# Kernel optimization log

Measured on AMD Instinct MI355X. Metric: run time of the kernel, lower is better.

## Reference

```python
import jax, jax.numpy as jnp
import numpy as np

H = 256          # hidden_channels
NP, NJ, NC = 8192, 8192, 4096  # person / job_posting / company node counts
EA, EW, EP = 262144, 131072, 131072  # edge counts per relation


def _gcn(x_src, W, b, edge_index, num_src, num_dst):
    """Bipartite GCNConv: h = x_src @ W; out[dst] = sum_e norm_e * h[src_e] + b,
    norm = deg_out(src)^-1/2 * deg_in(dst)^-1/2 (symmetric GCN normalization)."""
    h = x_src @ W                                # [num_src, H]
    row, col = edge_index[0], edge_index[1]
    ones = jnp.ones(row.shape[0], dtype=h.dtype)
    deg_src = jax.ops.segment_sum(ones, row, num_segments=num_src)
    deg_dst = jax.ops.segment_sum(ones, col, num_segments=num_dst)
    dis_src = jnp.where(deg_src > 0, jax.lax.rsqrt(jnp.maximum(deg_src, 1e-12)), 0.0)
    dis_dst = jnp.where(deg_dst > 0, jax.lax.rsqrt(jnp.maximum(deg_dst, 1e-12)), 0.0)
    norm = dis_src[row] * dis_dst[col]           # [E]
    out = jax.ops.segment_sum(h[row] * norm[:, None], col, num_segments=num_dst)
    return out + b


def setup_inputs() -> dict:
    key = jax.random.key(0)
    ks = jax.random.split(key, 12)
    s = 1.0 / np.sqrt(H)
    return {
        "x_person":  jax.random.normal(ks[0], (NP, H), jnp.float32),
        "x_job":     jax.random.normal(ks[1], (NJ, H), jnp.float32),
        "x_company": jax.random.normal(ks[2], (NC, H), jnp.float32),
        "ei_applied": jax.random.randint(ks[3], (2, EA), 0, 8192, jnp.int64 if jax.config.read('jax_enable_x64') else jnp.int32),
        "ei_worked":  jax.random.randint(ks[4], (2, EW), 0, 4096, jnp.int64 if jax.config.read('jax_enable_x64') else jnp.int32),
        "ei_posted":  jax.random.randint(ks[5], (2, EP), 0, 4096, jnp.int64 if jax.config.read('jax_enable_x64') else jnp.int32),
        "W_aj": jax.random.normal(ks[6], (H, H), jnp.float32) * s,
        "b_aj": jnp.zeros((H,), jnp.float32),
        "W_wa": jax.random.normal(ks[7], (H, H), jnp.float32) * s,
        "b_wa": jnp.zeros((H,), jnp.float32),
        "W_pb": jax.random.normal(ks[8], (H, H), jnp.float32) * s,
        "b_pb": jnp.zeros((H,), jnp.float32),
    }


def reference(x_person, x_job, x_company, ei_applied, ei_worked, ei_posted,
              W_aj, b_aj, W_wa, b_wa, W_pb, b_pb):
    Np, Nj, Nc = x_person.shape[0], x_job.shape[0], x_company.shape[0]
    # HeteroConv with aggr='sum': each dst type sums messages over its edge types
    job_emb = _gcn(x_person, W_aj, b_aj, ei_applied, Np, Nj)
    comp_emb = (_gcn(x_person, W_wa, b_wa, ei_worked, Np, Nc)
                + _gcn(x_job, W_pb, b_pb, ei_posted, Nj, Nc))  # computed but unused downstream
    del comp_emb
    person_emb = x_person  # 'person' is never a dst type; features pass through
    scores = jax.nn.sigmoid(person_emb @ job_emb.T)  # [Np, Nj]
    return scores
```

## Files before the change

### kernel.cpp

```cpp
#include <hip/hip_runtime.h>
#include <hip/hip_bf16.h>

#define HCH 256
#define NPN 8192
#define NJN 8192
#define EAE 262144
#define CAP 96

typedef _Float16 f16x8 __attribute__((ext_vector_type(8)));
typedef _Float16 f16x4 __attribute__((ext_vector_type(4)));
typedef float f32x4 __attribute__((ext_vector_type(4)));

typedef __attribute__((address_space(1))) void glb_void;
typedef __attribute__((address_space(3))) void lds_void;

#define WS_CUR   0
#define WS_DEG   32768
#define WS_CSR2  65536
#define WS_XH    3211264
#define WS_ZH    7405568
#define WS_GH    11599872
#define WS_WHT   15794176

__global__ void k_init(int* __restrict__ cnt, const float* __restrict__ W,
                       _Float16* __restrict__ WhT, const float* __restrict__ x,
                       _Float16* __restrict__ Xh) {
    int bid = blockIdx.x, t = threadIdx.x;
    if (bid < 64) {
        cnt[bid * 256 + t] = 0;
    } else if (bid < 320) {
        int idx = (bid - 64) * 256 + t;
        int n = idx >> 8, k = idx & 255;
        WhT[idx] = (_Float16)W[k * HCH + n];
    } else {
        int i = ((bid - 320) * 256 + t) * 4;
        float4 v = *(const float4*)(x + i);
        f16x4 h;
        h[0] = (_Float16)v.x; h[1] = (_Float16)v.y;
        h[2] = (_Float16)v.z; h[3] = (_Float16)v.w;
        *(f16x4*)(Xh + i) = h;
    }
}

__global__ void k_edge(const int* __restrict__ row, const int* __restrict__ col,
                       int* __restrict__ deg_src, int* __restrict__ cur,
                       int* __restrict__ csr2) {
    int e = blockIdx.x * 256 + threadIdx.x;
    int r = row[e], c = col[e];
    atomicAdd(&deg_src[r], 1);
    int p = atomicAdd(&cur[c], 1);
    if (p < CAP) csr2[c * CAP + p] = r;
}

__global__ __launch_bounds__(64)
void k_agg(const _Float16* __restrict__ Xh, const int* __restrict__ csr2,
           const int* __restrict__ cur, const int* __restrict__ deg_src,
           _Float16* __restrict__ Zh) {
    int j = blockIdx.x;
    int t = threadIdx.x;
    int degt = cur[j];
    int deg = degt > CAP ? CAP : degt;

    __shared__ int   sidx[CAP];
    __shared__ float sw[CAP];
    for (int b = t; b < deg; b += 64) {
        int s = csr2[j * CAP + b];
        sidx[b] = s;
        sw[b] = rsqrtf((float)deg_src[s]);
    }
    __syncthreads();

    float a0 = 0.f, a1 = 0.f, a2 = 0.f, a3 = 0.f;
    const _Float16* xb = Xh + t * 4;
    int e = 0;
    for (; e + 4 <= deg; e += 4) {
        int s0 = sidx[e], s1 = sidx[e + 1], s2 = sidx[e + 2], s3 = sidx[e + 3];
        float w0 = sw[e], w1 = sw[e + 1], w2 = sw[e + 2], w3 = sw[e + 3];
        f16x4 v0 = *(const f16x4*)(xb + (size_t)s0 * HCH);
        f16x4 v1 = *(const f16x4*)(xb + (size_t)s1 * HCH);
        f16x4 v2 = *(const f16x4*)(xb + (size_t)s2 * HCH);
        f16x4 v3 = *(const f16x4*)(xb + (size_t)s3 * HCH);
        a0 += w0 * (float)v0[0] + w1 * (float)v1[0] + w2 * (float)v2[0] + w3 * (float)v3[0];
        a1 += w0 * (float)v0[1] + w1 * (float)v1[1] + w2 * (float)v2[1] + w3 * (float)v3[1];
        a2 += w0 * (float)v0[2] + w1 * (float)v1[2] + w2 * (float)v2[2] + w3 * (float)v3[2];
        a3 += w0 * (float)v0[3] + w1 * (float)v1[3] + w2 * (float)v2[3] + w3 * (float)v3[3];
    }
    for (; e < deg; e++) {
        int s0 = sidx[e];
        float w0 = sw[e];
        f16x4 v0 = *(const f16x4*)(xb + (size_t)s0 * HCH);
        a0 += w0 * (float)v0[0]; a1 += w0 * (float)v0[1];
        a2 += w0 * (float)v0[2]; a3 += w0 * (float)v0[3];
    }
    f16x4 out;
    if (degt > 0) {
        float dd = rsqrtf((float)degt);
        out[0] = (_Float16)(a0 * dd); out[1] = (_Float16)(a1 * dd);
        out[2] = (_Float16)(a2 * dd); out[3] = (_Float16)(a3 * dd);
    } else {
        out[0] = out[1] = out[2] = out[3] = (_Float16)0.f;
    }
    *(f16x4*)(Zh + (size_t)j * HCH + t * 4) = out;
}

template <int TM, int TN>
__global__ __launch_bounds__(256, 2)
void k_gemm(const _Float16* __restrict__ A, const _Float16* __restrict__ Bt,
            const float* __restrict__ bias, _Float16* __restrict__ Cout, int Ncols) {
    constexpr int WM = TM / 2, WN = TN / 2;
    constexpr int MR = WM / 16, NR = WN / 16;
    constexpr int CHA = TM * 8 / 256;
    constexpr int CHB = TN * 8 / 256;
    constexpr int BOFF = TM * 128;

    __shared__ _Float16 sm[2][(TM + TN) * 64];

    int tid = threadIdx.x;
    int wid = tid >> 6, lane = tid & 63;

    int brow = blockIdx.y * TM;
    int bcol = blockIdx.x * TN;
    int wrow = (wid >> 1) * WM;
    int wcol = (wid & 1) * WN;

    f32x4 acc[MR][NR] = {};

    int lr = lane & 15;
    int kq = lane >> 4;

    auto stage = [&](int t, int b) {
        int k0 = t * 64;
#pragma unroll
        for (int i = 0; i < CHA; i++) {
            int wc0 = i * 256 + wid * 64;
            int c = wc0 + lane;
            int r = c >> 3, cc = c & 7;
            const char* ga = (const char*)A +
                (size_t)(brow + r) * (HCH * 2) + (size_t)(k0 + cc * 8) * 2;
            __builtin_amdgcn_global_load_lds(
                (glb_void*)ga, (lds_void*)((char*)sm[b] + wc0 * 16), 16, 0, 0);
        }
#pragma unroll
        for (int i = 0; i < CHB; i++) {
            int wc0 = i * 256 + wid * 64;
            int c = wc0 + lane;
            int r = c >> 3, cc = c & 7;
            const char* gb = (const char*)Bt +
                (size_t)(bcol + r) * (HCH * 2) + (size_t)(k0 + cc * 8) * 2;
            __builtin_amdgcn_global_load_lds(
                (glb_void*)gb, (lds_void*)((char*)sm[b] + BOFF + wc0 * 16), 16, 0, 0);
        }
    };

    stage(0, 0);
    __syncthreads();

    constexpr int NT = HCH / 64;
#pragma unroll
    for (int t = 0; t < NT; t++) {
        int cur = t & 1;
        if (t + 1 < NT) stage(t + 1, cur ^ 1);
        const char* base = (const char*)sm[cur];
#pragma unroll
        for (int kk = 0; kk < 64; kk += 32) {
            f16x8 af[MR], bfr[NR];
            int kbyte = (kk + kq * 8) * 2;
#pragma unroll
            for (int m = 0; m < MR; m++) {
                int r = wrow + m * 16 + lr;
                af[m] = *(const f16x8*)(base + r * 128 + kbyte);
            }
#pragma unroll
            for (int n = 0; n < NR; n++) {
                int r = wcol + n * 16 + lr;
                bfr[n] = *(const f16x8*)(base + BOFF + r * 128 + kbyte);
            }
#pragma unroll
            for (int m = 0; m < MR; m++)
#pragma unroll
                for (int n = 0; n < NR; n++)
                    acc[m][n] = __builtin_amdgcn_mfma_f32_16x16x32_f16(
                        af[m], bfr[n], acc[m][n], 0, 0, 0);
        }
        __syncthreads();
    }

    int rq = lane >> 4;
#pragma unroll
    for (int m = 0; m < MR; m++) {
#pragma unroll
        for (int n = 0; n < NR; n++) {
#pragma unroll
            for (int j = 0; j < 4; j++) {
                int gr = brow + wrow + m * 16 + rq * 4 + j;
                int gc = bcol + wcol + n * 16 + lr;
                float v = acc[m][n][j] + bias[gc];
                Cout[(size_t)gr * Ncols + gc] = (_Float16)v;
            }
        }
    }
}

#define G2_NW 32
__global__ __launch_bounds__(512, 1)
void k_gemm2(const _Float16* __restrict__ A, const _Float16* __restrict__ Bt,
             float* __restrict__ C) {
    __shared__ _Float16 smA[128 * HCH];
    __shared__ _Float16 smB[2][64 * HCH];
    __shared__ float    smC[128 * 64];

    int tid = threadIdx.x;
    int wid = tid >> 6, lane = tid & 63;
    int lr = lane & 15, kq = lane >> 4;

    int id = blockIdx.x;
    int xcd = id & 7, slot = id >> 3;
    int cg = xcd >> 1;
    int strip = slot + (xcd & 1) * 32;
    int brow = strip * 128;
    int bcol0 = cg * (64 * G2_NW);

    int wrow = (wid >> 1) * 32;
    int wcol = (wid & 1) * 32;

#pragma unroll
    for (int i = 0; i < 8; i++) {
        int wc0 = i * 512 + wid * 64;
        int c = wc0 + lane;
        int r = c >> 5, q = c & 31;
        int j = q ^ (r & 7);
        const char* ga = (const char*)(A + (size_t)(brow + r) * HCH + j * 8);
        __builtin_amdgcn_global_load_lds(
            (glb_void*)ga, (lds_void*)((char*)smA + wc0 * 16), 16, 0, 0);
    }
    auto stageB = [&](int t, int b) {
#pragma unroll
        for (int i = 0; i < 4; i++) {
            int wc0 = i * 512 + wid * 64;
            int c = wc0 + lane;
            int r = c >> 5, q = c & 31;
            int j = q ^ (r & 7);
            const char* gb = (const char*)(Bt +
                (size_t)(bcol0 + t * 64 + r) * HCH + j * 8);
            __builtin_amdgcn_global_load_lds(
                (glb_void*)gb, (lds_void*)((char*)smB[b] + wc0 * 16), 16, 0, 0);
        }
    };
    stageB(0, 0);
    __syncthreads();

    const char* sA = (const char*)smA;
    f16x8 areg[2][8];
#pragma unroll
    for (int m = 0; m < 2; m++) {
#pragma unroll
        for (int ks = 0; ks < 8; ks++) {
            int r = wrow + m * 16 + lr;
            int sb = ks * 4 + kq;
            areg[m][ks] = *(const f16x8*)(sA + r * 512 + ((sb ^ (r & 7)) << 4));
        }
    }

    for (int t = 0; t < G2_NW; t++) {
        int cb = t & 1;
        if (t + 1 < G2_NW) stageB(t + 1, cb ^ 1);
        __builtin_amdgcn_sched_barrier(0);
        const char* sB = (const char*)smB[cb];
        f32x4 acc[2][2] = {};
#pragma unroll
        for (int ks = 0; ks < 8; ks++) {
            f16x8 bf2[2];
            int sb = ks * 4 + kq;
#pragma unroll
            for (int n = 0; n < 2; n++) {
                int r = wcol + n * 16 + lr;
                bf2[n] = *(const f16x8*)(sB + r * 512 + ((sb ^ (r & 7)) << 4));
            }
#pragma unroll
            for (int m = 0; m < 2; m++)
#pragma unroll
                for (int n = 0; n < 2; n++)
                    acc[m][n] = __builtin_amdgcn_mfma_f32_16x16x32_f16(
                        bf2[n], areg[m][ks], acc[m][n], 0, 0, 0);
        }

#pragma unroll
        for (int m = 0; m < 2; m++) {
#pragma unroll
            for (int n = 0; n < 2; n++) {
                int row = wrow + m * 16 + lr;
                int ch = ((wcol + n * 16) >> 2) + kq;
                int sc = ch ^ (row & 7);
                *(f32x4*)(smC + row * 64 + sc * 4) = acc[m][n];
            }
        }
        asm volatile("s_waitcnt lgkmcnt(0)" ::: "memory");
        __builtin_amdgcn_s_barrier();
        __builtin_amdgcn_sched_barrier(0);

        int bcol = bcol0 + t * 64;
#pragma unroll
        for (int p = 0; p < 4; p++) {
            int flat = p * 512 + tid;
            int row = flat >> 4;
            int ch = flat & 15;
            int sc = ch ^ (row & 7);
            f32x4 v = *(const f32x4*)(smC + row * 64 + sc * 4);
            f32x4 o;
#pragma unroll
            for (int j = 0; j < 4; j++) {
                float e = __expf(-v[j]);
                o[j] = __builtin_amdgcn_rcpf(1.f + e);
            }
            __builtin_nontemporal_store(
                o, (f32x4*)(C + (size_t)(brow + row) * NJN + bcol + ch * 4));
        }

        if (t + 1 < G2_NW) {
            __builtin_amdgcn_sched_barrier(0);
            asm volatile("s_waitcnt vmcnt(4)" ::: "memory");
            __builtin_amdgcn_s_barrier();
            __builtin_amdgcn_sched_barrier(0);
        }
    }
}

extern "C" void kernel_launch(void* const* d_in, const int* in_sizes, int n_in,
                              void* d_out, int out_size, void* d_ws, size_t ws_size,
                              hipStream_t stream) {
    const float* x_person = (const float*)d_in[0];
    const int*   ei_app   = (const int*)d_in[3];
    const float* W_aj     = (const float*)d_in[6];
    const float* b_aj     = (const float*)d_in[7];

    const int* erow = ei_app;
    const int* ecol = ei_app + EAE;

    char* w = (char*)d_ws;
    int*      cur     = (int*)(w + WS_CUR);
    int*      deg_src = (int*)(w + WS_DEG);
    int*      csr2    = (int*)(w + WS_CSR2);
    _Float16* Xh      = (_Float16*)(w + WS_XH);
    _Float16* Zh      = (_Float16*)(w + WS_ZH);
    _Float16* Gh      = (_Float16*)(w + WS_GH);
    _Float16* WhT     = (_Float16*)(w + WS_WHT);

    k_init<<<2368, 256, 0, stream>>>(cur, W_aj, WhT, x_person, Xh);
    k_edge<<<EAE / 256, 256, 0, stream>>>(erow, ecol, deg_src, cur, csr2);
    k_agg<<<NJN, 64, 0, stream>>>(Xh, csr2, cur, deg_src, Zh);
    {
        dim3 grid(HCH / 128, NJN / 64);
        k_gemm<64, 128><<<grid, 256, 0, stream>>>(Zh, WhT, b_aj, Gh, HCH);
    }
    k_gemm2<<<256, 512, 0, stream>>>(Xh, Gh, (float*)d_out);
}
```

Baseline: 128.1 us.

## Shrink gemm2 LDS footprint and double grid to raise occupancy

```diff
diff --git a/kernel.cpp b/kernel.cpp
--- a/kernel.cpp
+++ b/kernel.cpp
@@ -201,12 +201,11 @@
     }
 }
 
-#define G2_NW 32
-__global__ __launch_bounds__(512, 1)
+#define G2_NT 16
+__global__ __launch_bounds__(512, 4)
 void k_gemm2(const _Float16* __restrict__ A, const _Float16* __restrict__ Bt,
              float* __restrict__ C) {
-    __shared__ _Float16 smA[128 * HCH];
-    __shared__ _Float16 smB[2][64 * HCH];
+    __shared__ _Float16 smB[64 * HCH];
     __shared__ float    smC[128 * 64];
 
     int tid = threadIdx.x;
@@ -214,26 +213,26 @@
     int lr = lane & 15, kq = lane >> 4;
 
     int id = blockIdx.x;
-    int xcd = id & 7, slot = id >> 3;
-    int cg = xcd >> 1;
-    int strip = slot + (xcd & 1) * 32;
+    int cg = id & 7;
+    int strip = id >> 3;
     int brow = strip * 128;
-    int bcol0 = cg * (64 * G2_NW);
+    int bcol0 = cg * (64 * G2_NT);
 
     int wrow = (wid >> 1) * 32;
     int wcol = (wid & 1) * 32;
 
-#pragma unroll
-    for (int i = 0; i < 8; i++) {
-        int wc0 = i * 512 + wid * 64;
-        int c = wc0 + lane;
-        int r = c >> 5, q = c & 31;
-        int j = q ^ (r & 7);
-        const char* ga = (const char*)(A + (size_t)(brow + r) * HCH + j * 8);
-        __builtin_amdgcn_global_load_lds(
-            (glb_void*)ga, (lds_void*)((char*)smA + wc0 * 16), 16, 0, 0);
-    }
-    auto stageB = [&](int t, int b) {
+    f16x8 areg[2][8];
+#pragma unroll
+    for (int m = 0; m < 2; m++) {
+#pragma unroll
+        for (int ks = 0; ks < 8; ks++) {
+            int r = brow + wrow + m * 16 + lr;
+            int sb = ks * 4 + kq;
+            areg[m][ks] = *(const f16x8*)(A + (size_t)r * HCH + sb * 8);
+        }
+    }
+
+    auto stageB = [&](int t) {
 #pragma unroll
         for (int i = 0; i < 4; i++) {
             int wc0 = i * 512 + wid * 64;
@@ -243,29 +242,14 @@
             const char* gb = (const char*)(Bt +
                 (size_t)(bcol0 + t * 64 + r) * HCH + j * 8);
             __builtin_amdgcn_global_load_lds(
-                (glb_void*)gb, (lds_void*)((char*)smB[b] + wc0 * 16), 16, 0, 0);
+                (glb_void*)gb, (lds_void*)((char*)smB + wc0 * 16), 16, 0, 0);
         }
     };
-    stageB(0, 0);
+    stageB(0);
     __syncthreads();
 
-    const char* sA = (const char*)smA;
-    f16x8 areg[2][8];
-#pragma unroll
-    for (int m = 0; m < 2; m++) {
-#pragma unroll
-        for (int ks = 0; ks < 8; ks++) {
-            int r = wrow + m * 16 + lr;
-            int sb = ks * 4 + kq;
-            areg[m][ks] = *(const f16x8*)(sA + r * 512 + ((sb ^ (r & 7)) << 4));
-        }
-    }
-
-    for (int t = 0; t < G2_NW; t++) {
-        int cb = t & 1;
-        if (t + 1 < G2_NW) stageB(t + 1, cb ^ 1);
-        __builtin_amdgcn_sched_barrier(0);
-        const char* sB = (const char*)smB[cb];
+    for (int t = 0; t < G2_NT; t++) {
+        const char* sB = (const char*)smB;
         f32x4 acc[2][2] = {};
 #pragma unroll
         for (int ks = 0; ks < 8; ks++) {
@@ -296,6 +280,9 @@
         }
         asm volatile("s_waitcnt lgkmcnt(0)" ::: "memory");
         __builtin_amdgcn_s_barrier();
+        __builtin_amdgcn_sched_barrier(0);
+
+        if (t + 1 < G2_NT) stageB(t + 1);
         __builtin_amdgcn_sched_barrier(0);
 
         int bcol = bcol0 + t * 64;
@@ -316,7 +303,7 @@
                 o, (f32x4*)(C + (size_t)(brow + row) * NJN + bcol + ch * 4));
         }
 
-        if (t + 1 < G2_NW) {
+        if (t + 1 < G2_NT) {
             __builtin_amdgcn_sched_barrier(0);
             asm volatile("s_waitcnt vmcnt(4)" ::: "memory");
             __builtin_amdgcn_s_barrier();
@@ -352,5 +339,5 @@
         dim3 grid(HCH / 128, NJN / 64);
         k_gemm<64, 128><<<grid, 256, 0, stream>>>(Zh, WhT, b_aj, Gh, HCH);
     }
-    k_gemm2<<<256, 512, 0, stream>>>(Xh, Gh, (float*)d_out);
-}
+    k_gemm2<<<512, 512, 0, stream>>>(Xh, Gh, (float*)d_out);
+}
```

Result: slower. 137.1 us (+7.0%).
